# Optimization experiments

Hardware: AMD Instinct MI355X
Metric: run time of the kernel (lower is better)

## Reference

```python
import jax, jax.numpy as jnp
import numpy as np

EMBED_DIM = 1024
NUM_HEADS = 16
HEAD_DIM = EMBED_DIM // NUM_HEADS
N, S = 4, 2048


def setup_inputs() -> dict:
    key = jax.random.key(0)
    ks = jax.random.split(key, 11)
    s = 1.0 / np.sqrt(EMBED_DIM)
    inp = {
        'query': jax.random.normal(ks[0], (N, S, EMBED_DIM), jnp.float32),
        'key': jax.random.normal(ks[1], (N, S, EMBED_DIM), jnp.float32),
        'value': jax.random.normal(ks[2], (N, S, EMBED_DIM), jnp.float32),
        'wq': jax.random.normal(ks[3], (EMBED_DIM, EMBED_DIM), jnp.float32) * s,
        'bq': jnp.zeros((EMBED_DIM,), jnp.float32),
        'wk': jax.random.normal(ks[4], (EMBED_DIM, EMBED_DIM), jnp.float32) * s,
        'bk': jnp.zeros((EMBED_DIM,), jnp.float32),
        'wv': jax.random.normal(ks[5], (EMBED_DIM, EMBED_DIM), jnp.float32) * s,
        'bv': jnp.zeros((EMBED_DIM,), jnp.float32),
        'wo': jax.random.normal(ks[6], (EMBED_DIM, EMBED_DIM), jnp.float32) * s,
        'bo': jnp.zeros((EMBED_DIM,), jnp.float32),
    }
    return inp


def reference(query, key, value, wq, bq, wk, bk, wv, bv, wo, bo):
    n = query.shape[0]
    # projections: y = x @ W^T + b (torch nn.Linear convention)
    Q = query @ wq.T + bq
    K = key @ wk.T + bk
    V = value @ wv.T + bv
    # [n, h, s, d]
    Q = Q.reshape(n, -1, NUM_HEADS, HEAD_DIM).transpose(0, 2, 1, 3)
    K = K.reshape(n, -1, NUM_HEADS, HEAD_DIM).transpose(0, 2, 1, 3)
    V = V.reshape(n, -1, NUM_HEADS, HEAD_DIM).transpose(0, 2, 1, 3)
    energy = jnp.einsum('nhqd,nhkd->nhqk', Q, K)
    attn = jax.nn.softmax(energy / jnp.sqrt(jnp.float32(HEAD_DIM)), axis=-1)
    out = jnp.einsum('nhqk,nhkd->nhqd', attn, V)
    out = out.transpose(0, 2, 1, 3).reshape(n, -1, NUM_HEADS * HEAD_DIM)
    return out @ wo.T + bo
```

## Files before the change

kernel.cpp:

```cpp
#include <hip/hip_runtime.h>
#include <hip/hip_bf16.h>

#define EMBED 1024
#define SEQ   2048
#define NB    4
#define NH    16
#define HD    64
#define MROWS (NB*SEQ)

typedef __attribute__((ext_vector_type(4))) float  f32x4;
typedef __attribute__((ext_vector_type(8))) short  s16x8;

#define MFMA16(a,b,c) __builtin_amdgcn_mfma_f32_16x16x32_bf16((a),(b),(c),0,0,0)

__device__ __forceinline__ unsigned short f2bf(float f) {
    union { float f; unsigned int u; } v; v.f = f;
    unsigned int r = v.u + 0x7fffu + ((v.u >> 16) & 1u);
    return (unsigned short)(r >> 16);
}
__device__ __forceinline__ unsigned int cvtpk(float a, float b) {
    unsigned int r;
    asm("v_cvt_pk_bf16_f32 %0, %1, %2" : "=v"(r) : "v"(a), "v"(b));
    return r;
}
__device__ __forceinline__ float exp2r(float x) {
    float r;
    asm("v_exp_f32 %0, %1" : "=v"(r) : "v"(x));
    return r;
}
__device__ __forceinline__ void gload16(const void* g, void* l) {
    __builtin_amdgcn_global_load_lds(
        (const __attribute__((address_space(1))) void*)g,
        (__attribute__((address_space(3))) void*)l, 16, 0, 0);
}

#define SC2 0.18033688f

__global__ __launch_bounds__(256) void qkv_fused(
    const float* __restrict__ Aq, const float* __restrict__ Ak,
    const float* __restrict__ Av,
    const float* __restrict__ wq, const float* __restrict__ wk,
    const float* __restrict__ wv,
    const float* __restrict__ bq, const float* __restrict__ bk,
    const float* __restrict__ bv,
    unsigned short* __restrict__ Qp, unsigned short* __restrict__ Kp,
    unsigned short* __restrict__ Vt)
{
    __shared__ unsigned short Ald[128*72];
    __shared__ unsigned short Bld[128*72];
    const int t   = threadIdx.x;
    const int bm  = blockIdx.x, bn = blockIdx.y;
    const int sel = bn >> 3, bnl = bn & 7;
    const float* Af   = sel == 0 ? Aq : (sel == 1 ? Ak : Av);
    const float* W    = sel == 0 ? wq : (sel == 1 ? wk : wv);
    const float* bias = sel == 0 ? bq : (sel == 1 ? bk : bv);

    const int wid = t >> 6, lane = t & 63, l15 = lane & 15, blk = lane >> 4;
    const int wr  = wid >> 1, wc = wid & 1;

    f32x4 acc[4][4] = {};

    for (int kt = 0; kt < EMBED/64; ++kt) {
        #pragma unroll
        for (int i = 0; i < 8; ++i) {
            int f = t + 256*i, row = f >> 4, c4 = f & 15;
            float4 v = *(const float4*)(Af + (size_t)(bm*128+row)*EMBED + kt*64 + c4*4);
            *(uint2*)&Ald[row*72 + c4*4] = make_uint2(cvtpk(v.x,v.y), cvtpk(v.z,v.w));
        }
        #pragma unroll
        for (int i = 0; i < 8; ++i) {
            int f = t + 256*i, row = f >> 4, c4 = f & 15;
            float4 v = *(const float4*)(W + (size_t)(bnl*128+row)*EMBED + kt*64 + c4*4);
            *(uint2*)&Bld[row*72 + c4*4] = make_uint2(cvtpk(v.x,v.y), cvtpk(v.z,v.w));
        }
        __syncthreads();
        #pragma unroll
        for (int ks = 0; ks < 2; ++ks) {
            s16x8 af[4], bf[4];
            #pragma unroll
            for (int mt = 0; mt < 4; ++mt)
                af[mt] = *(const s16x8*)&Ald[(wr*64 + mt*16 + l15)*72 + ks*32 + blk*8];
            #pragma unroll
            for (int nt = 0; nt < 4; ++nt)
                bf[nt] = *(const s16x8*)&Bld[(wc*64 + nt*16 + l15)*72 + ks*32 + blk*8];
            #pragma unroll
            for (int mt = 0; mt < 4; ++mt)
                #pragma unroll
                for (int nt = 0; nt < 4; ++nt)
                    acc[mt][nt] = MFMA16(af[mt], bf[nt], acc[mt][nt]);
        }
        __syncthreads();
    }

    const float scale = (sel == 0) ? SC2 : 1.0f;
    float bv4[4];
    #pragma unroll
    for (int nt = 0; nt < 4; ++nt)
        bv4[nt] = bias[bnl*128 + wc*64 + nt*16 + l15];

    #pragma unroll
    for (int mt = 0; mt < 4; ++mt) {
        #pragma unroll
        for (int nt = 0; nt < 4; ++nt) {
            const int m0 = bm*128 + wr*64 + mt*16 + blk*4;
            const int n  = bnl*128 + wc*64 + nt*16 + l15;
            f32x4 a = acc[mt][nt];
            if (sel < 2) {
                unsigned short* Yb = (sel == 0) ? Qp : Kp;
                #pragma unroll
                for (int r = 0; r < 4; ++r)
                    Yb[(size_t)(m0+r)*EMBED + n] = f2bf((a[r] + bv4[nt]) * scale);
            } else {
                const int b = m0 >> 11, s = m0 & (SEQ-1);
                const int h = n >> 6,  d = n & (HD-1);
                ushort4 pk;
                pk.x = f2bf(a[0] + bv4[nt]); pk.y = f2bf(a[1] + bv4[nt]);
                pk.z = f2bf(a[2] + bv4[nt]); pk.w = f2bf(a[3] + bv4[nt]);
                *(ushort4*)&Vt[(((size_t)b*NH + h)*HD + d)*SEQ + s] = pk;
            }
        }
    }
}

__global__ __launch_bounds__(256) void gemm_out(
    const unsigned short* __restrict__ Ab, const float* __restrict__ W,
    const float* __restrict__ bias, float* __restrict__ Yf)
{
    __shared__ unsigned short Ald[128*64];
    __shared__ unsigned short Bld[128*72];
    const int t   = threadIdx.x;
    const int bm  = blockIdx.x, bn = blockIdx.y;
    const int wid = t >> 6, lane = t & 63, l15 = lane & 15, blk = lane >> 4;
    const int wr  = wid >> 1, wc = wid & 1;

    f32x4 acc[4][4] = {};

    for (int kt = 0; kt < EMBED/64; ++kt) {
        #pragma unroll
        for (int i = 0; i < 4; ++i) {
            const int u = i*256 + t, row = u >> 3, slot = u & 7;
            const unsigned short* src = Ab + (size_t)(bm*128+row)*EMBED
                                           + kt*64 + (slot ^ (row & 7))*8;
            gload16(src, (char*)Ald + i*4096 + wid*1024);
        }
        #pragma unroll
        for (int i = 0; i < 8; ++i) {
            int f = t + 256*i, row = f >> 4, c4 = f & 15;
            float4 v = *(const float4*)(W + (size_t)(bn*128+row)*EMBED + kt*64 + c4*4);
            *(uint2*)&Bld[row*72 + c4*4] = make_uint2(cvtpk(v.x,v.y), cvtpk(v.z,v.w));
        }
        asm volatile("s_waitcnt vmcnt(0)" ::: "memory");
        __syncthreads();
        #pragma unroll
        for (int ks = 0; ks < 2; ++ks) {
            s16x8 af[4], bf[4];
            #pragma unroll
            for (int mt = 0; mt < 4; ++mt) {
                const int ra = wr*64 + mt*16 + l15;
                af[mt] = *(const s16x8*)((const char*)Ald + ra*128
                             + ((ks*64 + blk*16) ^ ((ra & 7) << 4)));
            }
            #pragma unroll
            for (int nt = 0; nt < 4; ++nt)
                bf[nt] = *(const s16x8*)&Bld[(wc*64 + nt*16 + l15)*72 + ks*32 + blk*8];
            #pragma unroll
            for (int mt = 0; mt < 4; ++mt)
                #pragma unroll
                for (int nt = 0; nt < 4; ++nt)
                    acc[mt][nt] = MFMA16(af[mt], bf[nt], acc[mt][nt]);
        }
        __syncthreads();
    }

    float bv4[4];
    #pragma unroll
    for (int nt = 0; nt < 4; ++nt)
        bv4[nt] = bias[bn*128 + wc*64 + nt*16 + l15];

    #pragma unroll
    for (int mt = 0; mt < 4; ++mt)
        #pragma unroll
        for (int nt = 0; nt < 4; ++nt) {
            const int m0 = bm*128 + wr*64 + mt*16 + blk*4;
            const int n  = bn*128 + wc*64 + nt*16 + l15;
            f32x4 a = acc[mt][nt];
            #pragma unroll
            for (int r = 0; r < 4; ++r)
                Yf[(size_t)(m0+r)*EMBED + n] = a[r] + bv4[nt];
        }
}

__global__ __launch_bounds__(512) void attn_fwd(
    const unsigned short* __restrict__ Qp,
    const unsigned short* __restrict__ Kp,
    const unsigned short* __restrict__ Vt,
    unsigned short* __restrict__ ctx)
{
    __shared__ unsigned short Kld[2][64*64];
    __shared__ unsigned short Vld[2][64*64];
    __shared__ unsigned short Pld[8][32*64];

    const int t = threadIdx.x, wid = t >> 6, lane = t & 63;
    const int l15 = lane & 15, blk = lane >> 4;
    const int bh = blockIdx.x, qb = blockIdx.y;
    const int b = bh >> 4, h = bh & (NH-1);
    const int q0 = qb*256 + wid*32;

    s16x8 qf[2][2];
    #pragma unroll
    for (int qs = 0; qs < 2; ++qs) {
        const unsigned short* qp = Qp + (size_t)(b*SEQ + q0 + qs*16 + l15)*EMBED + h*HD;
        qf[qs][0] = *(const s16x8*)(qp + blk*8);
        qf[qs][1] = *(const s16x8*)(qp + 32 + blk*8);
    }

    const unsigned short* kb = Kp + (size_t)b*SEQ*EMBED + h*HD;
    const unsigned short* vb = Vt + (size_t)bh*HD*SEQ;

    const int u  = wid*64 + lane;
    const int r0 = u >> 3;
    const int s0 = ((((u&7)<<4) ^ ((r0&7)<<4)) >> 1);
    const unsigned short* kS = kb + (size_t)r0*EMBED + s0;
    const unsigned short* vS = vb + (size_t)r0*SEQ  + s0;

    unsigned short* pl = &Pld[wid][0];
    const int rc0 = (blk*16) ^ ((l15 & 7) << 4);
    const int rc1 = rc0 ^ 64;

    s16x8 onesf;
    #pragma unroll
    for (int i = 0; i < 8; ++i) onesf[i] = (short)0x3F80;

    f32x4 o[2][4] = {};
    f32x4 sacc[2] = {};

    gload16(kS, (char*)Kld[0] + wid*1024);
    gload16(vS, (char*)Vld[0] + wid*1024);
    asm volatile("s_waitcnt vmcnt(0)" ::: "memory");
    __syncthreads();

    int cur = 0;
    for (int tt = 0; tt < SEQ/64; ++tt) {
        if (tt + 1 < SEQ/64) {
            const size_t ko = (size_t)(tt+1)*64;
            gload16(kS + ko*EMBED, (char*)Kld[cur^1] + wid*1024);
            gload16(vS + ko,       (char*)Vld[cur^1] + wid*1024);
        }

        const char* kbase = (const char*)Kld[cur];
        const char* vbase = (const char*)Vld[cur];

        f32x4 sc[2][4];
        #pragma unroll
        for (int qs = 0; qs < 2; ++qs)
            #pragma unroll
            for (int kt = 0; kt < 4; ++kt)
                sc[qs][kt] = f32x4{0.f,0.f,0.f,0.f};
        __builtin_amdgcn_s_setprio(1);
        #pragma unroll
        for (int kt = 0; kt < 4; ++kt) {
            const char* krow = kbase + (kt*16 + l15)*128;
            s16x8 ka0 = *(const s16x8*)(krow + rc0);
            s16x8 ka1 = *(const s16x8*)(krow + rc1);
            #pragma unroll
            for (int qs = 0; qs < 2; ++qs) {
                sc[qs][kt] = MFMA16(ka0, qf[qs][0], sc[qs][kt]);
                sc[qs][kt] = MFMA16(ka1, qf[qs][1], sc[qs][kt]);
            }
        }
        __builtin_amdgcn_s_setprio(0);

        #pragma unroll
        for (int qs = 0; qs < 2; ++qs) {
            #pragma unroll
            for (int kt = 0; kt < 4; ++kt) {
                const float e0 = exp2r(sc[qs][kt][0]);
                const float e1 = exp2r(sc[qs][kt][1]);
                const float e2 = exp2r(sc[qs][kt][2]);
                const float e3 = exp2r(sc[qs][kt][3]);
                const int off = (qs*16 + l15)*128 + ((kt*32 + blk*8) ^ ((l15 & 7) << 4));
                *(uint2*)((char*)pl + off) = make_uint2(cvtpk(e0,e1), cvtpk(e2,e3));
            }
        }

        s16x8 pa[2][2];
        #pragma unroll
        for (int qs = 0; qs < 2; ++qs) {
            const char* prow = (const char*)pl + (qs*16 + l15)*128;
            pa[qs][0] = *(const s16x8*)(prow + rc0);
            pa[qs][1] = *(const s16x8*)(prow + rc1);
        }
        __builtin_amdgcn_s_setprio(1);
        #pragma unroll
        for (int qs = 0; qs < 2; ++qs) {
            sacc[qs] = MFMA16(pa[qs][0], onesf, sacc[qs]);
            sacc[qs] = MFMA16(pa[qs][1], onesf, sacc[qs]);
        }
        #pragma unroll
        for (int dt = 0; dt < 4; ++dt) {
            const char* vrow = vbase + (dt*16 + l15)*128;
            s16x8 vb0 = *(const s16x8*)(vrow + rc0);
            s16x8 vb1 = *(const s16x8*)(vrow + rc1);
            #pragma unroll
            for (int qs = 0; qs < 2; ++qs) {
                o[qs][dt] = MFMA16(pa[qs][0], vb0, o[qs][dt]);
                o[qs][dt] = MFMA16(pa[qs][1], vb1, o[qs][dt]);
            }
        }
        __builtin_amdgcn_s_setprio(0);

        asm volatile("s_waitcnt vmcnt(0)" ::: "memory");
        __syncthreads();
        cur ^= 1;
    }

    #pragma unroll
    for (int qs = 0; qs < 2; ++qs) {
        float li[4];
        #pragma unroll
        for (int r = 0; r < 4; ++r) li[r] = 1.f / sacc[qs][r];
        unsigned short* cp = ctx + (size_t)(b*SEQ + q0 + qs*16)*EMBED + h*HD;
        #pragma unroll
        for (int dt = 0; dt < 4; ++dt)
            #pragma unroll
            for (int r = 0; r < 4; ++r)
                cp[(size_t)(blk*4 + r)*EMBED + dt*16 + l15] = f2bf(o[qs][dt][r] * li[r]);
    }
}

extern "C" void kernel_launch(void* const* d_in, const int* in_sizes, int n_in,
                              void* d_out, int out_size, void* d_ws, size_t ws_size,
                              hipStream_t stream)
{
    const float* q  = (const float*)d_in[0];
    const float* k  = (const float*)d_in[1];
    const float* v  = (const float*)d_in[2];
    const float* wq = (const float*)d_in[3];
    const float* bq = (const float*)d_in[4];
    const float* wk = (const float*)d_in[5];
    const float* bk = (const float*)d_in[6];
    const float* wv = (const float*)d_in[7];
    const float* bv = (const float*)d_in[8];
    const float* wo = (const float*)d_in[9];
    const float* bo = (const float*)d_in[10];

    unsigned short* Qp  = (unsigned short*)d_out;
    unsigned short* Kp  = Qp + (size_t)MROWS*EMBED;
    unsigned short* Vt  = (unsigned short*)d_ws;
    unsigned short* ctx = Vt + (size_t)MROWS*EMBED;
    float* out = (float*)d_out;

    qkv_fused<<<dim3(MROWS/128, 24), dim3(256), 0, stream>>>(
        q, k, v, wq, wk, wv, bq, bk, bv, Qp, Kp, Vt);
    attn_fwd<<<dim3(NB*NH, SEQ/256), dim3(512), 0, stream>>>(Qp, Kp, Vt, ctx);
    gemm_out<<<dim3(MROWS/128, EMBED/128), dim3(256), 0, stream>>>(ctx, wo, bo, out);
}
```

Before: 196.6 us.

## Pre-convert weights to bf16 once and load them into LDS directly

A new kernel converts the four fp32 weight matrices to bf16 once per call, folding the query scale into wq. The QKV and output GEMMs then fetch weight tiles with global_load_lds into swizzled LDS instead of reloading fp32 and converting in every block. This cuts weight bandwidth and conversion ALU work in the GEMMs, at the cost of an extra launch and an 8 MB workspace write. The new path runs only when the workspace is at least 40 MB, otherwise the old path runs.

```diff
diff --git a/kernel.cpp b/kernel.cpp
--- a/kernel.cpp
+++ b/kernel.cpp
@@ -7,6 +7,7 @@
 #define NH    16
 #define HD    64
 #define MROWS (NB*SEQ)
+#define WELEM (EMBED*EMBED)
 
 typedef __attribute__((ext_vector_type(4))) float  f32x4;
 typedef __attribute__((ext_vector_type(8))) short  s16x8;
@@ -36,23 +37,43 @@
 
 #define SC2 0.18033688f
 
+__global__ __launch_bounds__(256) void conv_w(
+    const float* __restrict__ wq, const float* __restrict__ wk,
+    const float* __restrict__ wv, const float* __restrict__ wo,
+    unsigned short* __restrict__ Wbf)
+{
+    const int i   = blockIdx.x*256 + threadIdx.x;
+    const int seg = i >> 17;
+    const int off = i & 131071;
+    const float* src = seg == 0 ? wq : (seg == 1 ? wk : (seg == 2 ? wv : wo));
+    const float sc   = seg == 0 ? SC2 : 1.f;
+    const float4 a = *(const float4*)(src + (size_t)off*8);
+    const float4 b = *(const float4*)(src + (size_t)off*8 + 4);
+    uint4 o;
+    o.x = cvtpk(a.x*sc, a.y*sc); o.y = cvtpk(a.z*sc, a.w*sc);
+    o.z = cvtpk(b.x*sc, b.y*sc); o.w = cvtpk(b.z*sc, b.w*sc);
+    *(uint4*)(Wbf + (size_t)seg*WELEM + (size_t)off*8) = o;
+}
+
+template<int WMODE>
 __global__ __launch_bounds__(256) void qkv_fused(
     const float* __restrict__ Aq, const float* __restrict__ Ak,
     const float* __restrict__ Av,
     const float* __restrict__ wq, const float* __restrict__ wk,
-    const float* __restrict__ wv,
+    const float* __restrict__ wv, const unsigned short* __restrict__ Wbf,
     const float* __restrict__ bq, const float* __restrict__ bk,
     const float* __restrict__ bv,
     unsigned short* __restrict__ Qp, unsigned short* __restrict__ Kp,
     unsigned short* __restrict__ Vt)
 {
     __shared__ unsigned short Ald[128*72];
-    __shared__ unsigned short Bld[128*72];
+    __shared__ unsigned short Bld[WMODE ? 128*64 : 128*72];
     const int t   = threadIdx.x;
     const int bm  = blockIdx.x, bn = blockIdx.y;
     const int sel = bn >> 3, bnl = bn & 7;
     const float* Af   = sel == 0 ? Aq : (sel == 1 ? Ak : Av);
-    const float* W    = sel == 0 ? wq : (sel == 1 ? wk : wv);
+    const float* Wf   = sel == 0 ? wq : (sel == 1 ? wk : wv);
+    const unsigned short* Wb = Wbf + (size_t)sel*WELEM;
     const float* bias = sel == 0 ? bq : (sel == 1 ? bk : bv);
 
     const int wid = t >> 6, lane = t & 63, l15 = lane & 15, blk = lane >> 4;
@@ -61,17 +82,30 @@
     f32x4 acc[4][4] = {};
 
     for (int kt = 0; kt < EMBED/64; ++kt) {
+        if (WMODE == 1) {
+            #pragma unroll
+            for (int i = 0; i < 4; ++i) {
+                const int u = i*256 + t, row = u >> 3, slot = u & 7;
+                const unsigned short* src = Wb + (size_t)(bnl*128+row)*EMBED
+                                               + kt*64 + (slot ^ (row & 7))*8;
+                gload16(src, (char*)Bld + i*4096 + wid*1024);
+            }
+        }
         #pragma unroll
         for (int i = 0; i < 8; ++i) {
             int f = t + 256*i, row = f >> 4, c4 = f & 15;
             float4 v = *(const float4*)(Af + (size_t)(bm*128+row)*EMBED + kt*64 + c4*4);
             *(uint2*)&Ald[row*72 + c4*4] = make_uint2(cvtpk(v.x,v.y), cvtpk(v.z,v.w));
         }
-        #pragma unroll
-        for (int i = 0; i < 8; ++i) {
-            int f = t + 256*i, row = f >> 4, c4 = f & 15;
-            float4 v = *(const float4*)(W + (size_t)(bnl*128+row)*EMBED + kt*64 + c4*4);
-            *(uint2*)&Bld[row*72 + c4*4] = make_uint2(cvtpk(v.x,v.y), cvtpk(v.z,v.w));
+        if (WMODE == 0) {
+            #pragma unroll
+            for (int i = 0; i < 8; ++i) {
+                int f = t + 256*i, row = f >> 4, c4 = f & 15;
+                float4 v = *(const float4*)(Wf + (size_t)(bnl*128+row)*EMBED + kt*64 + c4*4);
+                *(uint2*)&Bld[row*72 + c4*4] = make_uint2(cvtpk(v.x,v.y), cvtpk(v.z,v.w));
+            }
+        } else {
+            asm volatile("s_waitcnt vmcnt(0)" ::: "memory");
         }
         __syncthreads();
         #pragma unroll
@@ -81,8 +115,14 @@
             for (int mt = 0; mt < 4; ++mt)
                 af[mt] = *(const s16x8*)&Ald[(wr*64 + mt*16 + l15)*72 + ks*32 + blk*8];
             #pragma unroll
-            for (int nt = 0; nt < 4; ++nt)
-                bf[nt] = *(const s16x8*)&Bld[(wc*64 + nt*16 + l15)*72 + ks*32 + blk*8];
+            for (int nt = 0; nt < 4; ++nt) {
+                const int rb = wc*64 + nt*16 + l15;
+                if (WMODE == 1)
+                    bf[nt] = *(const s16x8*)((const char*)Bld + rb*128
+                                 + ((ks*64 + blk*16) ^ ((rb & 7) << 4)));
+                else
+                    bf[nt] = *(const s16x8*)&Bld[rb*72 + ks*32 + blk*8];
+            }
             #pragma unroll
             for (int mt = 0; mt < 4; ++mt)
                 #pragma unroll
@@ -95,8 +135,10 @@
     const float scale = (sel == 0) ? SC2 : 1.0f;
     float bv4[4];
     #pragma unroll
-    for (int nt = 0; nt < 4; ++nt)
-        bv4[nt] = bias[bnl*128 + wc*64 + nt*16 + l15];
+    for (int nt = 0; nt < 4; ++nt) {
+        float bb = bias[bnl*128 + wc*64 + nt*16 + l15];
+        bv4[nt] = (WMODE == 1) ? bb*scale : bb;
+    }
 
     #pragma unroll
     for (int mt = 0; mt < 4; ++mt) {
@@ -108,8 +150,11 @@
             if (sel < 2) {
                 unsigned short* Yb = (sel == 0) ? Qp : Kp;
                 #pragma unroll
-                for (int r = 0; r < 4; ++r)
-                    Yb[(size_t)(m0+r)*EMBED + n] = f2bf((a[r] + bv4[nt]) * scale);
+                for (int r = 0; r < 4; ++r) {
+                    float val = (WMODE == 1) ? (a[r] + bv4[nt])
+                                             : (a[r] + bv4[nt]) * scale;
+                    Yb[(size_t)(m0+r)*EMBED + n] = f2bf(val);
+                }
             } else {
                 const int b = m0 >> 11, s = m0 & (SEQ-1);
                 const int h = n >> 6,  d = n & (HD-1);
@@ -122,12 +167,14 @@
     }
 }
 
+template<int WMODE>
 __global__ __launch_bounds__(256) void gemm_out(
     const unsigned short* __restrict__ Ab, const float* __restrict__ W,
+    const unsigned short* __restrict__ Wb,
     const float* __restrict__ bias, float* __restrict__ Yf)
 {
     __shared__ unsigned short Ald[128*64];
-    __shared__ unsigned short Bld[128*72];
+    __shared__ unsigned short Bld[WMODE ? 128*64 : 128*72];
     const int t   = threadIdx.x;
     const int bm  = blockIdx.x, bn = blockIdx.y;
     const int wid = t >> 6, lane = t & 63, l15 = lane & 15, blk = lane >> 4;
@@ -143,11 +190,21 @@
                                            + kt*64 + (slot ^ (row & 7))*8;
             gload16(src, (char*)Ald + i*4096 + wid*1024);
         }
-        #pragma unroll
-        for (int i = 0; i < 8; ++i) {
-            int f = t + 256*i, row = f >> 4, c4 = f & 15;
-            float4 v = *(const float4*)(W + (size_t)(bn*128+row)*EMBED + kt*64 + c4*4);
-            *(uint2*)&Bld[row*72 + c4*4] = make_uint2(cvtpk(v.x,v.y), cvtpk(v.z,v.w));
+        if (WMODE == 1) {
+            #pragma unroll
+            for (int i = 0; i < 4; ++i) {
+                const int u = i*256 + t, row = u >> 3, slot = u & 7;
+                const unsigned short* src = Wb + (size_t)(bn*128+row)*EMBED
+                                               + kt*64 + (slot ^ (row & 7))*8;
+                gload16(src, (char*)Bld + i*4096 + wid*1024);
+            }
+        } else {
+            #pragma unroll
+            for (int i = 0; i < 8; ++i) {
+                int f = t + 256*i, row = f >> 4, c4 = f & 15;
+                float4 v = *(const float4*)(W + (size_t)(bn*128+row)*EMBED + kt*64 + c4*4);
+                *(uint2*)&Bld[row*72 + c4*4] = make_uint2(cvtpk(v.x,v.y), cvtpk(v.z,v.w));
+            }
         }
         asm volatile("s_waitcnt vmcnt(0)" ::: "memory");
         __syncthreads();
@@ -161,8 +218,14 @@
                              + ((ks*64 + blk*16) ^ ((ra & 7) << 4)));
             }
             #pragma unroll
-            for (int nt = 0; nt < 4; ++nt)
-                bf[nt] = *(const s16x8*)&Bld[(wc*64 + nt*16 + l15)*72 + ks*32 + blk*8];
+            for (int nt = 0; nt < 4; ++nt) {
+                const int rb = wc*64 + nt*16 + l15;
+                if (WMODE == 1)
+                    bf[nt] = *(const s16x8*)((const char*)Bld + rb*128
+                                 + ((ks*64 + blk*16) ^ ((rb & 7) << 4)));
+                else
+                    bf[nt] = *(const s16x8*)&Bld[rb*72 + ks*32 + blk*8];
+            }
             #pragma unroll
             for (int mt = 0; mt < 4; ++mt)
                 #pragma unroll
@@ -348,10 +411,26 @@
     unsigned short* Kp  = Qp + (size_t)MROWS*EMBED;
     unsigned short* Vt  = (unsigned short*)d_ws;
     unsigned short* ctx = Vt + (size_t)MROWS*EMBED;
+    unsigned short* Wbf = ctx + (size_t)MROWS*EMBED;
     float* out = (float*)d_out;
 
-    qkv_fused<<<dim3(MROWS/128, 24), dim3(256), 0, stream>>>(
-        q, k, v, wq, wk, wv, bq, bk, bv, Qp, Kp, Vt);
+    const bool pre = ws_size >= (size_t)40*1024*1024;
+
+    dim3 tpb(256);
+    if (pre) {
+        conv_w<<<2048, tpb, 0, stream>>>(wq, wk, wv, wo, Wbf);
+        qkv_fused<1><<<dim3(MROWS/128, 24), tpb, 0, stream>>>(
+            q, k, v, wq, wk, wv, Wbf, bq, bk, bv, Qp, Kp, Vt);
+    } else {
+        qkv_fused<0><<<dim3(MROWS/128, 24), tpb, 0, stream>>>(
+            q, k, v, wq, wk, wv, Wbf, bq, bk, bv, Qp, Kp, Vt);
+    }
     attn_fwd<<<dim3(NB*NH, SEQ/256), dim3(512), 0, stream>>>(Qp, Kp, Vt, ctx);
-    gemm_out<<<dim3(MROWS/128, EMBED/128), dim3(256), 0, stream>>>(ctx, wo, bo, out);
-}
+    if (pre) {
+        gemm_out<1><<<dim3(MROWS/128, EMBED/128), tpb, 0, stream>>>(
+            ctx, wo, Wbf + (size_t)3*WELEM, bo, out);
+    } else {
+        gemm_out<0><<<dim3(MROWS/128, EMBED/128), tpb, 0, stream>>>(
+            ctx, wo, Wbf, bo, out);
+    }
+}
```

New measurement: 182.3 us. 1.08x faster.
